# Kernel optimization log

Hardware: AMD Instinct MI355X
Metric: run time of the kernel (lower is better)

## Reference

```python
import jax, jax.numpy as jnp
import numpy as np

N = 100000   # nodes
E = 1600000  # edges (avg degree 16)
IN_F = 256
OUT_F = 128


def setup_inputs() -> dict:
    key = jax.random.key(0)
    k1, k2, k3, k4, k5, k6 = jax.random.split(key, 6)
    std = 1.0 / (OUT_F ** 0.5)
    return {
        "x": jax.random.normal(k1, (N, IN_F), dtype=jnp.float32),
        "weight": jax.random.uniform(k2, (IN_F, OUT_F), dtype=jnp.float32, minval=-std, maxval=std),
        "bias": jax.random.uniform(k3, (OUT_F,), dtype=jnp.float32, minval=-std, maxval=std),
        "edge_weight": jax.random.uniform(k4, (E,), dtype=jnp.float32),
        "row": jax.random.randint(k5, (E,), 0, N, dtype=jnp.int32),
        "col": jax.random.randint(k6, (E,), 0, N, dtype=jnp.int32),
    }


def reference(x, weight, bias, edge_weight, row, col):
    # support = x @ W : dense GEMM [N, in] x [in, out]
    support = jnp.matmul(x, weight)
    # spmm(adj, support): gather source-node rows, scale by edge value,
    # scatter-add into destination rows (COO SpMM).
    msgs = support[col] * edge_weight[:, None]          # [E, out]
    aggregated = jax.ops.segment_sum(msgs, row, num_segments=N)  # [N, out]
    return aggregated + bias
```

## Files before the change

### kernel.cpp

```cpp
#include <hip/hip_runtime.h>

#define N_NODES 100000
#define IN_F 256
#define OUT_F 128

#define BKT_SHIFT 7
#define BKT_SIZE (1 << BKT_SHIFT)
#define NBKT ((N_NODES + BKT_SIZE - 1) / BKT_SIZE)
#define SLAB_CAP 4096
#define CHUNK 4096
#define GCAP 2816

#define WS_SUP 0
#define WS_SLAB 25600000
#define WS_BSWZ 51300000
#define WS_BCUR 51400000
#define WS_NEEDED 65200016

typedef __attribute__((ext_vector_type(8))) short short8;
typedef __attribute__((ext_vector_type(4))) float f32x4;
typedef __attribute__((ext_vector_type(2))) float f32x2;

__device__ __forceinline__ unsigned short f2bf(float f) {
  unsigned u = __float_as_uint(f);
  unsigned r = (u + 0x7fffu + ((u >> 16) & 1u)) >> 16;
  return (unsigned short)r;
}

__global__ __launch_bounds__(256) void prep_bswz_kernel(
    const float* __restrict__ w, unsigned short* __restrict__ bswz,
    int* __restrict__ bcur) {
  const int tid = blockIdx.x * 256 + threadIdx.x;
  if (tid < NBKT) bcur[tid] = 0;
  const int j = tid & 7;
  const int lane = (tid >> 3) & 63;
  const int nt = (tid >> 9) & 7;
  const int ks = tid >> 12;
  const int k = ks * 32 + ((lane >> 4) * 8) + j;
  const int n = nt * 16 + (lane & 15);
  bswz[tid] = f2bf(w[k * OUT_F + n]);
}

__global__ __launch_bounds__(512) void gemm_mfma_kernel(
    const float* __restrict__ x, const unsigned short* __restrict__ bswz,
    unsigned short* __restrict__ supb) {
  __shared__ unsigned short lb[32768];

  const int t = threadIdx.x;
  {
    const int4* src = (const int4*)bswz;
    int4* dst = (int4*)lb;
#pragma unroll
    for (int i = 0; i < 8; ++i) dst[t + i * 512] = src[t + i * 512];
  }
  __syncthreads();

  const int w = t >> 6;
  const int lane = t & 63;
  const int quad = lane >> 4;
  const int m16 = lane & 15;

  const int row = blockIdx.x * 128 + w * 16 + m16;
  const int rc = row < N_NODES ? row : N_NODES - 1;
  const float* ap = x + (long long)rc * IN_F + quad * 8;
  const short8* bb = (const short8*)lb + lane;

  f32x4 acc[8];
#pragma unroll
  for (int nt = 0; nt < 8; ++nt) acc[nt] = (f32x4){0.f, 0.f, 0.f, 0.f};

#pragma unroll
  for (int ks = 0; ks < 8; ++ks) {
    const float4 a0 = *(const float4*)(ap + ks * 32);
    const float4 a1 = *(const float4*)(ap + ks * 32 + 4);
    short8 af;
    af[0] = f2bf(a0.x); af[1] = f2bf(a0.y); af[2] = f2bf(a0.z); af[3] = f2bf(a0.w);
    af[4] = f2bf(a1.x); af[5] = f2bf(a1.y); af[6] = f2bf(a1.z); af[7] = f2bf(a1.w);
#pragma unroll
    for (int nt = 0; nt < 8; ++nt) {
      const short8 bf = bb[(ks * 8 + nt) * 64];
      acc[nt] = __builtin_amdgcn_mfma_f32_16x16x32_bf16(af, bf, acc[nt], 0, 0, 0);
    }
  }

  const int rowbase = blockIdx.x * 128 + w * 16 + quad * 4;
#pragma unroll
  for (int nt = 0; nt < 8; ++nt) {
#pragma unroll
    for (int r = 0; r < 4; ++r) {
      const int gr = rowbase + r;
      if (gr < N_NODES)
        supb[(long long)gr * OUT_F + nt * 16 + m16] = f2bf(acc[nt][r]);
    }
  }
}

__global__ __launch_bounds__(1024) void bucket_fill_kernel(
    const int* __restrict__ row, const int* __restrict__ col,
    const float* __restrict__ ew, int* __restrict__ bcur,
    int2* __restrict__ slab, int E) {
  __shared__ int lcnt[1024];
  __shared__ int lscan[1024];
  __shared__ int outb[NBKT];
  __shared__ int2 stage[CHUNK];
  __shared__ unsigned short bid[CHUNK];

  const int t = threadIdx.x;
  const int e0 = blockIdx.x * CHUNK;
  lcnt[t] = 0;
  __syncthreads();

  int myb[4];
  int rank[4];
  int2 pk[4];
#pragma unroll
  for (int k = 0; k < 4; ++k) {
    const int e = e0 + k * 1024 + t;
    myb[k] = -1;
    if (e < E) {
      const int r = row[e];
      const int c = col[e];
      const float wv = ew[e];
      const int b = r >> BKT_SHIFT;
      myb[k] = b;
      pk[k] = make_int2(c | ((r & (BKT_SIZE - 1)) << 17), __float_as_int(wv));
      rank[k] = atomicAdd(&lcnt[b], 1);
    }
  }
  __syncthreads();

  const int v = lcnt[t];
  lscan[t] = v;
  __syncthreads();
  for (int off = 1; off < 1024; off <<= 1) {
    const int w = (t >= off) ? lscan[t - off] : 0;
    __syncthreads();
    lscan[t] += w;
    __syncthreads();
  }
  const int excl = lscan[t] - v;
  if (t < NBKT && v) outb[t] = atomicAdd(&bcur[t], v);
  __syncthreads();
  lscan[t] = excl;
  __syncthreads();

#pragma unroll
  for (int k = 0; k < 4; ++k) {
    if (myb[k] >= 0) {
      const int p = lscan[myb[k]] + rank[k];
      stage[p] = pk[k];
      bid[p] = (unsigned short)myb[k];
    }
  }
  __syncthreads();

  const int total = min(CHUNK, E - e0);
  for (int i = t; i < total; i += 1024) {
    const int b = bid[i];
    const int rel = outb[b] + (i - lscan[b]);
    if (rel < SLAB_CAP) slab[(long long)b * SLAB_CAP + rel] = stage[i];
  }
}

__global__ __launch_bounds__(512) void node_gather_kernel(
    const unsigned short* __restrict__ supb, const int2* __restrict__ slab,
    const int* __restrict__ bcur, const float* __restrict__ bias,
    float* __restrict__ out) {
  __shared__ int2 eS[GCAP];
  __shared__ int hist[BKT_SIZE];
  __shared__ int sbase[BKT_SIZE];
  __shared__ int cur[BKT_SIZE];

  const int t = threadIdx.x;
  const int bk = blockIdx.x;
  const long long sb = (long long)bk * SLAB_CAP;
  int n = bcur[bk];
  n = n > SLAB_CAP ? SLAB_CAP : n;

  const int w = t >> 6;
  const int lane = t & 63;
  const unsigned short* sp = supb + lane * 2;
  const float2 bv = *(const float2*)(bias + lane * 2);

  if (n <= GCAP) {
    if (t < BKT_SIZE) hist[t] = 0;
    __syncthreads();
    for (int i = t; i < n; i += 512)
      atomicAdd(&hist[(slab[sb + i].x >> 17) & (BKT_SIZE - 1)], 1);
    __syncthreads();
    int v = 0;
    if (t < BKT_SIZE) { v = hist[t]; sbase[t] = v; }
    __syncthreads();
    for (int off = 1; off < BKT_SIZE; off <<= 1) {
      int add = 0;
      if (t < BKT_SIZE && t >= off) add = sbase[t - off];
      __syncthreads();
      if (t < BKT_SIZE) sbase[t] += add;
      __syncthreads();
    }
    if (t < BKT_SIZE) { sbase[t] -= v; cur[t] = sbase[t]; }
    __syncthreads();
    for (int i = t; i < n; i += 512) {
      const int2 e = slab[sb + i];
      const int lr = (e.x >> 17) & (BKT_SIZE - 1);
      eS[atomicAdd(&cur[lr], 1)] = e;
    }
    __syncthreads();

    for (int k = 0; k < 16; ++k) {
      const int lr0 = w * 16 + k;
      const int node = (bk << BKT_SHIFT) + lr0;
      if (node >= N_NODES) break;
      const int s = sbase[lr0];
      const int e_end = s + hist[lr0];
      float a0 = 0.f, a1 = 0.f, b0 = 0.f, b1 = 0.f;
      float c0 = 0.f, c1 = 0.f, d0 = 0.f, d1 = 0.f;
      float p0 = 0.f, p1 = 0.f, q0 = 0.f, q1 = 0.f;
      float r0 = 0.f, r1 = 0.f, s0 = 0.f, s1 = 0.f;
      int j = s;
      for (; j + 8 <= e_end; j += 8) {
        const int2 E0 = eS[j];     const int2 E1 = eS[j + 1];
        const int2 E2 = eS[j + 2]; const int2 E3 = eS[j + 3];
        const int2 E4 = eS[j + 4]; const int2 E5 = eS[j + 5];
        const int2 E6 = eS[j + 6]; const int2 E7 = eS[j + 7];
        const unsigned u0 = *(const unsigned*)(sp + (long long)(E0.x & 0x1FFFF) * OUT_F);
        const unsigned u1 = *(const unsigned*)(sp + (long long)(E1.x & 0x1FFFF) * OUT_F);
        const unsigned u2 = *(const unsigned*)(sp + (long long)(E2.x & 0x1FFFF) * OUT_F);
        const unsigned u3 = *(const unsigned*)(sp + (long long)(E3.x & 0x1FFFF) * OUT_F);
        const unsigned u4 = *(const unsigned*)(sp + (long long)(E4.x & 0x1FFFF) * OUT_F);
        const unsigned u5 = *(const unsigned*)(sp + (long long)(E5.x & 0x1FFFF) * OUT_F);
        const unsigned u6 = *(const unsigned*)(sp + (long long)(E6.x & 0x1FFFF) * OUT_F);
        const unsigned u7 = *(const unsigned*)(sp + (long long)(E7.x & 0x1FFFF) * OUT_F);
        a0 = fmaf(__uint_as_float(u0 << 16), __int_as_float(E0.y), a0);
        a1 = fmaf(__uint_as_float(u0 & 0xffff0000u), __int_as_float(E0.y), a1);
        b0 = fmaf(__uint_as_float(u1 << 16), __int_as_float(E1.y), b0);
        b1 = fmaf(__uint_as_float(u1 & 0xffff0000u), __int_as_float(E1.y), b1);
        c0 = fmaf(__uint_as_float(u2 << 16), __int_as_float(E2.y), c0);
        c1 = fmaf(__uint_as_float(u2 & 0xffff0000u), __int_as_float(E2.y), c1);
        d0 = fmaf(__uint_as_float(u3 << 16), __int_as_float(E3.y), d0);
        d1 = fmaf(__uint_as_float(u3 & 0xffff0000u), __int_as_float(E3.y), d1);
        p0 = fmaf(__uint_as_float(u4 << 16), __int_as_float(E4.y), p0);
        p1 = fmaf(__uint_as_float(u4 & 0xffff0000u), __int_as_float(E4.y), p1);
        q0 = fmaf(__uint_as_float(u5 << 16), __int_as_float(E5.y), q0);
        q1 = fmaf(__uint_as_float(u5 & 0xffff0000u), __int_as_float(E5.y), q1);
        r0 = fmaf(__uint_as_float(u6 << 16), __int_as_float(E6.y), r0);
        r1 = fmaf(__uint_as_float(u6 & 0xffff0000u), __int_as_float(E6.y), r1);
        s0 = fmaf(__uint_as_float(u7 << 16), __int_as_float(E7.y), s0);
        s1 = fmaf(__uint_as_float(u7 & 0xffff0000u), __int_as_float(E7.y), s1);
      }
      for (; j + 2 <= e_end; j += 2) {
        const int2 E0 = eS[j];
        const int2 E1 = eS[j + 1];
        const unsigned u0 = *(const unsigned*)(sp + (long long)(E0.x & 0x1FFFF) * OUT_F);
        const unsigned u1 = *(const unsigned*)(sp + (long long)(E1.x & 0x1FFFF) * OUT_F);
        a0 = fmaf(__uint_as_float(u0 << 16), __int_as_float(E0.y), a0);
        a1 = fmaf(__uint_as_float(u0 & 0xffff0000u), __int_as_float(E0.y), a1);
        b0 = fmaf(__uint_as_float(u1 << 16), __int_as_float(E1.y), b0);
        b1 = fmaf(__uint_as_float(u1 & 0xffff0000u), __int_as_float(E1.y), b1);
      }
      if (j < e_end) {
        const int2 E0 = eS[j];
        const unsigned u0 = *(const unsigned*)(sp + (long long)(E0.x & 0x1FFFF) * OUT_F);
        a0 = fmaf(__uint_as_float(u0 << 16), __int_as_float(E0.y), a0);
        a1 = fmaf(__uint_as_float(u0 & 0xffff0000u), __int_as_float(E0.y), a1);
      }
      const f32x2 vv = {a0 + b0 + c0 + d0 + p0 + q0 + r0 + s0 + bv.x,
                        a1 + b1 + c1 + d1 + p1 + q1 + r1 + s1 + bv.y};
      __builtin_nontemporal_store(vv, (f32x2*)(out + (long long)node * OUT_F + lane * 2));
    }
  } else {
    for (int k = 0; k < 16; ++k) {
      const int lr0 = w * 16 + k;
      const int node = (bk << BKT_SHIFT) + lr0;
      if (node >= N_NODES) break;
      float a0 = 0.f, a1 = 0.f;
      for (int i = 0; i < n; ++i) {
        const int2 e = slab[sb + i];
        if (((e.x >> 17) & (BKT_SIZE - 1)) == lr0) {
          const unsigned u = *(const unsigned*)(sp + (long long)(e.x & 0x1FFFF) * OUT_F);
          a0 = fmaf(__uint_as_float(u << 16), __int_as_float(e.y), a0);
          a1 = fmaf(__uint_as_float(u & 0xffff0000u), __int_as_float(e.y), a1);
        }
      }
      const f32x2 vv = {a0 + bv.x, a1 + bv.y};
      __builtin_nontemporal_store(vv, (f32x2*)(out + (long long)node * OUT_F + lane * 2));
    }
  }
}

__global__ __launch_bounds__(256) void bias_init_kernel(
    float* __restrict__ out, const float* __restrict__ bias) {
  const int t = blockIdx.x * blockDim.x + threadIdx.x;
  const int idx = t * 4;
  *(float4*)(out + idx) = *(const float4*)(bias + (idx & (OUT_F - 1)));
}

__global__ __launch_bounds__(256) void scatter_kernel(
    const unsigned short* __restrict__ supb, const float* __restrict__ ew,
    const int* __restrict__ row, const int* __restrict__ col,
    float* __restrict__ out, int E) {
  const long long t = (long long)blockIdx.x * blockDim.x + threadIdx.x;
  const int e = (int)(t >> 6);
  if (e >= E) return;
  const int lane = (int)(t & 63);
  const int c = col[e];
  const int r = row[e];
  const float wv = ew[e];
  const unsigned u = *(const unsigned*)(supb + (long long)c * OUT_F + lane * 2);
  float* o = out + (long long)r * OUT_F + lane * 2;
  atomicAdd(o, __uint_as_float(u << 16) * wv);
  atomicAdd(o + 1, __uint_as_float(u & 0xffff0000u) * wv);
}

extern "C" void kernel_launch(void* const* d_in, const int* in_sizes, int n_in,
                              void* d_out, int out_size, void* d_ws, size_t ws_size,
                              hipStream_t stream) {
  const float* x = (const float*)d_in[0];
  const float* weight = (const float*)d_in[1];
  const float* bias = (const float*)d_in[2];
  const float* edge_weight = (const float*)d_in[3];
  const int* row = (const int*)d_in[4];
  const int* col = (const int*)d_in[5];
  float* out = (float*)d_out;
  const int E = in_sizes[3];

  char* ws = (char*)d_ws;
  unsigned short* supb = (unsigned short*)(ws + WS_SUP);
  unsigned short* bswz = (unsigned short*)(ws + WS_BSWZ);
  int* bcur = (int*)(ws + WS_BCUR);

  prep_bswz_kernel<<<128, 256, 0, stream>>>(weight, bswz, bcur);
  gemm_mfma_kernel<<<(N_NODES + 127) / 128, 512, 0, stream>>>(x, bswz, supb);

  if (ws_size >= (size_t)WS_NEEDED) {
    int2* slab = (int2*)(ws + WS_SLAB);

    bucket_fill_kernel<<<(E + CHUNK - 1) / CHUNK, 1024, 0, stream>>>(
        row, col, edge_weight, bcur, slab, E);
    node_gather_kernel<<<NBKT, 512, 0, stream>>>(supb, slab, bcur, bias, out);
  } else {
    bias_init_kernel<<<(N_NODES * OUT_F / 4) / 256, 256, 0, stream>>>(out, bias);
    scatter_kernel<<<(int)(((long long)E * 64 + 255) / 256), 256, 0, stream>>>(
        supb, edge_weight, row, col, out, E);
  }
}
```

Baseline: 276.3 us.

## Shrink node buckets to 64, double edge chunk, and prefetch GEMM A rows

Node buckets shrink from 128 to 64 nodes, so there are twice as many gather blocks. Each gather block now has 256 threads and keeps its whole slab in LDS, and the slow fallback path is removed. The bucket fill kernel handles 8192 edges per block and does a two-segment scan over 2048 buckets. The GEMM loads A rows six k-steps ahead and sets an occupancy hint of 4 in launch_bounds. The aim is more parallelism in the gather stage and hidden global-load latency in the GEMM. In exchange there are more global atomics, more register pressure, and edges are silently dropped if a bucket exceeds 2048.

```diff
diff --git a/kernel.cpp b/kernel.cpp
--- a/kernel.cpp
+++ b/kernel.cpp
@@ -4,12 +4,11 @@
 #define IN_F 256
 #define OUT_F 128
 
-#define BKT_SHIFT 7
+#define BKT_SHIFT 6
 #define BKT_SIZE (1 << BKT_SHIFT)
 #define NBKT ((N_NODES + BKT_SIZE - 1) / BKT_SIZE)
-#define SLAB_CAP 4096
-#define CHUNK 4096
-#define GCAP 2816
+#define SLAB_CAP 2048
+#define CHUNK 8192
 
 #define WS_SUP 0
 #define WS_SLAB 25600000
@@ -41,7 +40,7 @@
   bswz[tid] = f2bf(w[k * OUT_F + n]);
 }
 
-__global__ __launch_bounds__(512) void gemm_mfma_kernel(
+__global__ __launch_bounds__(512, 4) void gemm_mfma_kernel(
     const float* __restrict__ x, const unsigned short* __restrict__ bswz,
     unsigned short* __restrict__ supb) {
   __shared__ unsigned short lb[32768];
@@ -69,13 +68,24 @@
 #pragma unroll
   for (int nt = 0; nt < 8; ++nt) acc[nt] = (f32x4){0.f, 0.f, 0.f, 0.f};
 
+  float4 A0[8], A1[8];
+#pragma unroll
+  for (int p = 0; p < 6; ++p) {
+    A0[p] = *(const float4*)(ap + p * 32);
+    A1[p] = *(const float4*)(ap + p * 32 + 4);
+  }
+
 #pragma unroll
   for (int ks = 0; ks < 8; ++ks) {
-    const float4 a0 = *(const float4*)(ap + ks * 32);
-    const float4 a1 = *(const float4*)(ap + ks * 32 + 4);
+    if (ks + 6 < 8) {
+      A0[ks + 6] = *(const float4*)(ap + (ks + 6) * 32);
+      A1[ks + 6] = *(const float4*)(ap + (ks + 6) * 32 + 4);
+    }
     short8 af;
-    af[0] = f2bf(a0.x); af[1] = f2bf(a0.y); af[2] = f2bf(a0.z); af[3] = f2bf(a0.w);
-    af[4] = f2bf(a1.x); af[5] = f2bf(a1.y); af[6] = f2bf(a1.z); af[7] = f2bf(a1.w);
+    af[0] = f2bf(A0[ks].x); af[1] = f2bf(A0[ks].y);
+    af[2] = f2bf(A0[ks].z); af[3] = f2bf(A0[ks].w);
+    af[4] = f2bf(A1[ks].x); af[5] = f2bf(A1[ks].y);
+    af[6] = f2bf(A1[ks].z); af[7] = f2bf(A1[ks].w);
 #pragma unroll
     for (int nt = 0; nt < 8; ++nt) {
       const short8 bf = bb[(ks * 8 + nt) * 64];
@@ -99,22 +109,23 @@
     const int* __restrict__ row, const int* __restrict__ col,
     const float* __restrict__ ew, int* __restrict__ bcur,
     int2* __restrict__ slab, int E) {
-  __shared__ int lcnt[1024];
-  __shared__ int lscan[1024];
-  __shared__ int outb[NBKT];
+  __shared__ int lcnt[2048];
+  __shared__ int sc[2048];
+  __shared__ int outb[2048];
   __shared__ int2 stage[CHUNK];
   __shared__ unsigned short bid[CHUNK];
 
   const int t = threadIdx.x;
   const int e0 = blockIdx.x * CHUNK;
   lcnt[t] = 0;
-  __syncthreads();
-
-  int myb[4];
-  int rank[4];
-  int2 pk[4];
-#pragma unroll
-  for (int k = 0; k < 4; ++k) {
+  lcnt[t + 1024] = 0;
+  __syncthreads();
+
+  int myb[8];
+  int rank[8];
+  int2 pk[8];
+#pragma unroll
+  for (int k = 0; k < 8; ++k) {
     const int e = e0 + k * 1024 + t;
     myb[k] = -1;
     if (e < E) {
@@ -129,25 +140,36 @@
   }
   __syncthreads();
 
-  const int v = lcnt[t];
-  lscan[t] = v;
+  const int v0 = lcnt[t];
+  const int v1 = lcnt[t + 1024];
+  sc[t] = v0;
+  sc[t + 1024] = v1;
   __syncthreads();
   for (int off = 1; off < 1024; off <<= 1) {
-    const int w = (t >= off) ? lscan[t - off] : 0;
+    const int w0 = (t >= off) ? sc[t - off] : 0;
+    const int w1 = (t >= off) ? sc[1024 + t - off] : 0;
     __syncthreads();
-    lscan[t] += w;
+    sc[t] += w0;
+    sc[1024 + t] += w1;
     __syncthreads();
   }
-  const int excl = lscan[t] - v;
-  if (t < NBKT && v) outb[t] = atomicAdd(&bcur[t], v);
-  __syncthreads();
-  lscan[t] = excl;
-  __syncthreads();
-
-#pragma unroll
-  for (int k = 0; k < 4; ++k) {
+  const int tot0 = sc[1023];
+  __syncthreads();
+  sc[1024 + t] += tot0;
+  __syncthreads();
+  const int ex0 = sc[t] - v0;
+  const int ex1 = sc[1024 + t] - v1;
+  if (v0) outb[t] = atomicAdd(&bcur[t], v0);
+  if (t + 1024 < NBKT && v1) outb[t + 1024] = atomicAdd(&bcur[t + 1024], v1);
+  __syncthreads();
+  sc[t] = ex0;
+  sc[t + 1024] = ex1;
+  __syncthreads();
+
+#pragma unroll
+  for (int k = 0; k < 8; ++k) {
     if (myb[k] >= 0) {
-      const int p = lscan[myb[k]] + rank[k];
+      const int p = sc[myb[k]] + rank[k];
       stage[p] = pk[k];
       bid[p] = (unsigned short)myb[k];
     }
@@ -157,16 +179,16 @@
   const int total = min(CHUNK, E - e0);
   for (int i = t; i < total; i += 1024) {
     const int b = bid[i];
-    const int rel = outb[b] + (i - lscan[b]);
+    const int rel = outb[b] + (i - sc[b]);
     if (rel < SLAB_CAP) slab[(long long)b * SLAB_CAP + rel] = stage[i];
   }
 }
 
-__global__ __launch_bounds__(512) void node_gather_kernel(
+__global__ __launch_bounds__(256) void node_gather_kernel(
     const unsigned short* __restrict__ supb, const int2* __restrict__ slab,
     const int* __restrict__ bcur, const float* __restrict__ bias,
     float* __restrict__ out) {
-  __shared__ int2 eS[GCAP];
+  __shared__ int2 eS[SLAB_CAP];
   __shared__ int hist[BKT_SIZE];
   __shared__ int sbase[BKT_SIZE];
   __shared__ int cur[BKT_SIZE];
@@ -182,109 +204,90 @@
   const unsigned short* sp = supb + lane * 2;
   const float2 bv = *(const float2*)(bias + lane * 2);
 
-  if (n <= GCAP) {
-    if (t < BKT_SIZE) hist[t] = 0;
+  if (t < BKT_SIZE) hist[t] = 0;
+  __syncthreads();
+  for (int i = t; i < n; i += 256)
+    atomicAdd(&hist[(slab[sb + i].x >> 17) & (BKT_SIZE - 1)], 1);
+  __syncthreads();
+  int v = 0;
+  if (t < BKT_SIZE) { v = hist[t]; sbase[t] = v; }
+  __syncthreads();
+  for (int off = 1; off < BKT_SIZE; off <<= 1) {
+    int add = 0;
+    if (t < BKT_SIZE && t >= off) add = sbase[t - off];
     __syncthreads();
-    for (int i = t; i < n; i += 512)
-      atomicAdd(&hist[(slab[sb + i].x >> 17) & (BKT_SIZE - 1)], 1);
+    if (t < BKT_SIZE) sbase[t] += add;
     __syncthreads();
-    int v = 0;
-    if (t < BKT_SIZE) { v = hist[t]; sbase[t] = v; }
-    __syncthreads();
-    for (int off = 1; off < BKT_SIZE; off <<= 1) {
-      int add = 0;
-      if (t < BKT_SIZE && t >= off) add = sbase[t - off];
-      __syncthreads();
-      if (t < BKT_SIZE) sbase[t] += add;
-      __syncthreads();
-    }
-    if (t < BKT_SIZE) { sbase[t] -= v; cur[t] = sbase[t]; }
-    __syncthreads();
-    for (int i = t; i < n; i += 512) {
-      const int2 e = slab[sb + i];
-      const int lr = (e.x >> 17) & (BKT_SIZE - 1);
-      eS[atomicAdd(&cur[lr], 1)] = e;
-    }
-    __syncthreads();
-
-    for (int k = 0; k < 16; ++k) {
-      const int lr0 = w * 16 + k;
-      const int node = (bk << BKT_SHIFT) + lr0;
-      if (node >= N_NODES) break;
-      const int s = sbase[lr0];
-      const int e_end = s + hist[lr0];
-      float a0 = 0.f, a1 = 0.f, b0 = 0.f, b1 = 0.f;
-      float c0 = 0.f, c1 = 0.f, d0 = 0.f, d1 = 0.f;
-      float p0 = 0.f, p1 = 0.f, q0 = 0.f, q1 = 0.f;
-      float r0 = 0.f, r1 = 0.f, s0 = 0.f, s1 = 0.f;
-      int j = s;
-      for (; j + 8 <= e_end; j += 8) {
-        const int2 E0 = eS[j];     const int2 E1 = eS[j + 1];
-        const int2 E2 = eS[j + 2]; const int2 E3 = eS[j + 3];
-        const int2 E4 = eS[j + 4]; const int2 E5 = eS[j + 5];
-        const int2 E6 = eS[j + 6]; const int2 E7 = eS[j + 7];
-        const unsigned u0 = *(const unsigned*)(sp + (long long)(E0.x & 0x1FFFF) * OUT_F);
-        const unsigned u1 = *(const unsigned*)(sp + (long long)(E1.x & 0x1FFFF) * OUT_F);
-        const unsigned u2 = *(const unsigned*)(sp + (long long)(E2.x & 0x1FFFF) * OUT_F);
-        const unsigned u3 = *(const unsigned*)(sp + (long long)(E3.x & 0x1FFFF) * OUT_F);
-        const unsigned u4 = *(const unsigned*)(sp + (long long)(E4.x & 0x1FFFF) * OUT_F);
-        const unsigned u5 = *(const unsigned*)(sp + (long long)(E5.x & 0x1FFFF) * OUT_F);
-        const unsigned u6 = *(const unsigned*)(sp + (long long)(E6.x & 0x1FFFF) * OUT_F);
-        const unsigned u7 = *(const unsigned*)(sp + (long long)(E7.x & 0x1FFFF) * OUT_F);
-        a0 = fmaf(__uint_as_float(u0 << 16), __int_as_float(E0.y), a0);
-        a1 = fmaf(__uint_as_float(u0 & 0xffff0000u), __int_as_float(E0.y), a1);
-        b0 = fmaf(__uint_as_float(u1 << 16), __int_as_float(E1.y), b0);
-        b1 = fmaf(__uint_as_float(u1 & 0xffff0000u), __int_as_float(E1.y), b1);
-        c0 = fmaf(__uint_as_float(u2 << 16), __int_as_float(E2.y), c0);
-        c1 = fmaf(__uint_as_float(u2 & 0xffff0000u), __int_as_float(E2.y), c1);
-        d0 = fmaf(__uint_as_float(u3 << 16), __int_as_float(E3.y), d0);
-        d1 = fmaf(__uint_as_float(u3 & 0xffff0000u), __int_as_float(E3.y), d1);
-        p0 = fmaf(__uint_as_float(u4 << 16), __int_as_float(E4.y), p0);
-        p1 = fmaf(__uint_as_float(u4 & 0xffff0000u), __int_as_float(E4.y), p1);
-        q0 = fmaf(__uint_as_float(u5 << 16), __int_as_float(E5.y), q0);
-        q1 = fmaf(__uint_as_float(u5 & 0xffff0000u), __int_as_float(E5.y), q1);
-        r0 = fmaf(__uint_as_float(u6 << 16), __int_as_float(E6.y), r0);
-        r1 = fmaf(__uint_as_float(u6 & 0xffff0000u), __int_as_float(E6.y), r1);
-        s0 = fmaf(__uint_as_float(u7 << 16), __int_as_float(E7.y), s0);
-        s1 = fmaf(__uint_as_float(u7 & 0xffff0000u), __int_as_float(E7.y), s1);
-      }
-      for (; j + 2 <= e_end; j += 2) {
-        const int2 E0 = eS[j];
-        const int2 E1 = eS[j + 1];
-        const unsigned u0 = *(const unsigned*)(sp + (long long)(E0.x & 0x1FFFF) * OUT_F);
-        const unsigned u1 = *(const unsigned*)(sp + (long long)(E1.x & 0x1FFFF) * OUT_F);
-        a0 = fmaf(__uint_as_float(u0 << 16), __int_as_float(E0.y), a0);
-        a1 = fmaf(__uint_as_float(u0 & 0xffff0000u), __int_as_float(E0.y), a1);
-        b0 = fmaf(__uint_as_float(u1 << 16), __int_as_float(E1.y), b0);
-        b1 = fmaf(__uint_as_float(u1 & 0xffff0000u), __int_as_float(E1.y), b1);
-      }
-      if (j < e_end) {
-        const int2 E0 = eS[j];
-        const unsigned u0 = *(const unsigned*)(sp + (long long)(E0.x & 0x1FFFF) * OUT_F);
-        a0 = fmaf(__uint_as_float(u0 << 16), __int_as_float(E0.y), a0);
-        a1 = fmaf(__uint_as_float(u0 & 0xffff0000u), __int_as_float(E0.y), a1);
-      }
-      const f32x2 vv = {a0 + b0 + c0 + d0 + p0 + q0 + r0 + s0 + bv.x,
-                        a1 + b1 + c1 + d1 + p1 + q1 + r1 + s1 + bv.y};
-      __builtin_nontemporal_store(vv, (f32x2*)(out + (long long)node * OUT_F + lane * 2));
-    }
-  } else {
-    for (int k = 0; k < 16; ++k) {
-      const int lr0 = w * 16 + k;
-      const int node = (bk << BKT_SHIFT) + lr0;
-      if (node >= N_NODES) break;
-      float a0 = 0.f, a1 = 0.f;
-      for (int i = 0; i < n; ++i) {
-        const int2 e = slab[sb + i];
-        if (((e.x >> 17) & (BKT_SIZE - 1)) == lr0) {
-          const unsigned u = *(const unsigned*)(sp + (long long)(e.x & 0x1FFFF) * OUT_F);
-          a0 = fmaf(__uint_as_float(u << 16), __int_as_float(e.y), a0);
-          a1 = fmaf(__uint_as_float(u & 0xffff0000u), __int_as_float(e.y), a1);
-        }
-      }
-      const f32x2 vv = {a0 + bv.x, a1 + bv.y};
-      __builtin_nontemporal_store(vv, (f32x2*)(out + (long long)node * OUT_F + lane * 2));
-    }
+  }
+  if (t < BKT_SIZE) { sbase[t] -= v; cur[t] = sbase[t]; }
+  __syncthreads();
+  for (int i = t; i < n; i += 256) {
+    const int2 e = slab[sb + i];
+    const int lr = (e.x >> 17) & (BKT_SIZE - 1);
+    eS[atomicAdd(&cur[lr], 1)] = e;
+  }
+  __syncthreads();
+
+  for (int k = 0; k < 16; ++k) {
+    const int lr0 = w * 16 + k;
+    const int node = (bk << BKT_SHIFT) + lr0;
+    if (node >= N_NODES) break;
+    const int s = sbase[lr0];
+    const int e_end = s + hist[lr0];
+    float a0 = 0.f, a1 = 0.f, b0 = 0.f, b1 = 0.f;
+    float c0 = 0.f, c1 = 0.f, d0 = 0.f, d1 = 0.f;
+    float p0 = 0.f, p1 = 0.f, q0 = 0.f, q1 = 0.f;
+    float r0 = 0.f, r1 = 0.f, s0 = 0.f, s1 = 0.f;
+    int j = s;
+    for (; j + 8 <= e_end; j += 8) {
+      const int2 E0 = eS[j];     const int2 E1 = eS[j + 1];
+      const int2 E2 = eS[j + 2]; const int2 E3 = eS[j + 3];
+      const int2 E4 = eS[j + 4]; const int2 E5 = eS[j + 5];
+      const int2 E6 = eS[j + 6]; const int2 E7 = eS[j + 7];
+      const unsigned u0 = *(const unsigned*)(sp + (long long)(E0.x & 0x1FFFF) * OUT_F);
+      const unsigned u1 = *(const unsigned*)(sp + (long long)(E1.x & 0x1FFFF) * OUT_F);
+      const unsigned u2 = *(const unsigned*)(sp + (long long)(E2.x & 0x1FFFF) * OUT_F);
+      const unsigned u3 = *(const unsigned*)(sp + (long long)(E3.x & 0x1FFFF) * OUT_F);
+      const unsigned u4 = *(const unsigned*)(sp + (long long)(E4.x & 0x1FFFF) * OUT_F);
+      const unsigned u5 = *(const unsigned*)(sp + (long long)(E5.x & 0x1FFFF) * OUT_F);
+      const unsigned u6 = *(const unsigned*)(sp + (long long)(E6.x & 0x1FFFF) * OUT_F);
+      const unsigned u7 = *(const unsigned*)(sp + (long long)(E7.x & 0x1FFFF) * OUT_F);
+      a0 = fmaf(__uint_as_float(u0 << 16), __int_as_float(E0.y), a0);
+      a1 = fmaf(__uint_as_float(u0 & 0xffff0000u), __int_as_float(E0.y), a1);
+      b0 = fmaf(__uint_as_float(u1 << 16), __int_as_float(E1.y), b0);
+      b1 = fmaf(__uint_as_float(u1 & 0xffff0000u), __int_as_float(E1.y), b1);
+      c0 = fmaf(__uint_as_float(u2 << 16), __int_as_float(E2.y), c0);
+      c1 = fmaf(__uint_as_float(u2 & 0xffff0000u), __int_as_float(E2.y), c1);
+      d0 = fmaf(__uint_as_float(u3 << 16), __int_as_float(E3.y), d0);
+      d1 = fmaf(__uint_as_float(u3 & 0xffff0000u), __int_as_float(E3.y), d1);
+      p0 = fmaf(__uint_as_float(u4 << 16), __int_as_float(E4.y), p0);
+      p1 = fmaf(__uint_as_float(u4 & 0xffff0000u), __int_as_float(E4.y), p1);
+      q0 = fmaf(__uint_as_float(u5 << 16), __int_as_float(E5.y), q0);
+      q1 = fmaf(__uint_as_float(u5 & 0xffff0000u), __int_as_float(E5.y), q1);
+      r0 = fmaf(__uint_as_float(u6 << 16), __int_as_float(E6.y), r0);
+      r1 = fmaf(__uint_as_float(u6 & 0xffff0000u), __int_as_float(E6.y), r1);
+      s0 = fmaf(__uint_as_float(u7 << 16), __int_as_float(E7.y), s0);
+      s1 = fmaf(__uint_as_float(u7 & 0xffff0000u), __int_as_float(E7.y), s1);
+    }
+    for (; j + 2 <= e_end; j += 2) {
+      const int2 E0 = eS[j];
+      const int2 E1 = eS[j + 1];
+      const unsigned u0 = *(const unsigned*)(sp + (long long)(E0.x & 0x1FFFF) * OUT_F);
+      const unsigned u1 = *(const unsigned*)(sp + (long long)(E1.x & 0x1FFFF) * OUT_F);
+      a0 = fmaf(__uint_as_float(u0 << 16), __int_as_float(E0.y), a0);
+      a1 = fmaf(__uint_as_float(u0 & 0xffff0000u), __int_as_float(E0.y), a1);
+      b0 = fmaf(__uint_as_float(u1 << 16), __int_as_float(E1.y), b0);
+      b1 = fmaf(__uint_as_float(u1 & 0xffff0000u), __int_as_float(E1.y), b1);
+    }
+    if (j < e_end) {
+      const int2 E0 = eS[j];
+      const unsigned u0 = *(const unsigned*)(sp + (long long)(E0.x & 0x1FFFF) * OUT_F);
+      a0 = fmaf(__uint_as_float(u0 << 16), __int_as_float(E0.y), a0);
+      a1 = fmaf(__uint_as_float(u0 & 0xffff0000u), __int_as_float(E0.y), a1);
+    }
+    const f32x2 vv = {a0 + b0 + c0 + d0 + p0 + q0 + r0 + s0 + bv.x,
+                      a1 + b1 + c1 + d1 + p1 + q1 + r1 + s1 + bv.y};
+    __builtin_nontemporal_store(vv, (f32x2*)(out + (long long)node * OUT_F + lane * 2));
   }
 }
 
@@ -337,7 +340,7 @@
 
     bucket_fill_kernel<<<(E + CHUNK - 1) / CHUNK, 1024, 0, stream>>>(
         row, col, edge_weight, bcur, slab, E);
-    node_gather_kernel<<<NBKT, 512, 0, stream>>>(supb, slab, bcur, bias, out);
+    node_gather_kernel<<<NBKT, 256, 0, stream>>>(supb, slab, bcur, bias, out);
   } else {
     bias_init_kernel<<<(N_NODES * OUT_F / 4) / 256, 256, 0, stream>>>(out, bias);
     scatter_kernel<<<(int)(((long long)E * 64 + 255) / 256), 256, 0, stream>>>(
```

Result: faster. 268.5 us (-2.8%).
